# Optimization experiments

Measured on AMD Instinct MI355X. Metric: run time of the kernel, lower is better.

The kernel has to match this reference:

```python
import jax, jax.numpy as jnp
import numpy as np

B, S, D = 8, 2048, 512
H, LAT, OUT = 8, 64, 64


def setup_inputs() -> dict:
    key = jax.random.key(0)
    ks = jax.random.split(key, 5)
    return {
        "x": jax.random.normal(ks[0], (B, S, D), dtype=jnp.float32),
        "WQ": jax.random.normal(ks[1], (H, D, LAT), dtype=jnp.float32) * 0.05,
        "WK": jax.random.normal(ks[2], (H, D, LAT), dtype=jnp.float32) * 0.05,
        "WV": jax.random.normal(ks[3], (H, D, OUT), dtype=jnp.float32) * 0.05,
        "WO": jax.random.normal(ks[4], (H * OUT, OUT), dtype=jnp.float32) * 0.05,
    }


def reference(x, WQ, WK, WV, WO):
    # Per-head projections, vectorized over heads (faithful to the TF python loop).
    Q = jnp.einsum('bsd,hdk->bhsk', x, WQ)   # [B,H,S,LAT]
    K = jnp.einsum('bsd,hdk->bhsk', x, WK)   # [B,H,S,LAT]
    V = jnp.einsum('bsd,hdo->bhso', x, WV)   # [B,H,S,OUT]
    scale = jnp.asarray(1.0 / np.sqrt(LAT), dtype=x.dtype)
    A = jnp.einsum('bhqk,bhsk->bhqs', Q, K) * scale  # [B,H,S,S]
    A = jax.nn.softmax(A, axis=-1)
    O = jnp.einsum('bhqs,bhso->bhqo', A, V)  # [B,H,S,OUT]
    # concat heads along last axis (head 0 first, matching the TF loop order)
    O = jnp.transpose(O, (0, 2, 1, 3)).reshape(x.shape[0], x.shape[1], H * OUT)
    return O @ WO  # [B,S,OUT]
```

## Files before the change

### kernel.cpp

```cpp
#include <hip/hip_runtime.h>
#include <hip/hip_bf16.h>
#include <math.h>

static constexpr int Bn = 8, Sn = 2048, Dn = 512, Hn = 8, LATn = 64, OUTn = 64;

typedef short  bf16x8 __attribute__((ext_vector_type(8)));
typedef float  f32x4  __attribute__((ext_vector_type(4)));

__device__ __forceinline__ unsigned short f2bf(float f) {
    union { float f; unsigned int i; } v; v.f = f;
    unsigned int x = v.i;
    return (unsigned short)((x + 0x7FFFu + ((x >> 16) & 1u)) >> 16);
}
__device__ __forceinline__ unsigned int pack2bf(float a, float b) {
    unsigned int ua = __float_as_uint(a) + 0x8000u;
    unsigned int ub = __float_as_uint(b) + 0x8000u;
    return (ua >> 16) | (ub & 0xFFFF0000u);
}

#if __has_builtin(__builtin_amdgcn_exp2f)
#define EXP2(x) __builtin_amdgcn_exp2f(x)
#else
#define EXP2(x) exp2f(x)
#endif

__device__ __forceinline__ void gl_lds16(const void* g, void* l) {
    __builtin_amdgcn_global_load_lds(
        (const __attribute__((address_space(1))) unsigned int*)g,
        (__attribute__((address_space(3))) unsigned int*)l, 16, 0, 0);
}

__global__ __launch_bounds__(256) void wprep(
    const float* __restrict__ WQ, const float* __restrict__ WK,
    const float* __restrict__ WV, const float* __restrict__ WO,
    unsigned short* __restrict__ WT)
{
    __shared__ float tile[64][65];
    const int t  = threadIdx.x;
    const int d0 = blockIdx.x * 64;
    const int yy = blockIdx.y;

    const float* W; float scale = 1.0f; size_t dstbase;
    if (yy < 24) {
        int h = yy / 3, which = yy % 3;
        W = (which == 0) ? WQ : (which == 1) ? WK : WV;
        W += (size_t)h * Dn * 64;
        if (which == 0) scale = 0.125f * 1.44269504088896f;
        dstbase = ((size_t)h * 192 + which * 64) * Dn;
    } else {
        W = WO;
        dstbase = (size_t)8 * 192 * Dn;
    }

    for (int i = 0; i < 4; ++i) {
        int idx = i * 256 + t;
        int r = idx >> 4, c = (idx & 15) * 4;
        float4 u = *(const float4*)(W + (size_t)(d0 + r) * 64 + c);
        tile[r][c] = u.x; tile[r][c+1] = u.y; tile[r][c+2] = u.z; tile[r][c+3] = u.w;
    }
    __syncthreads();
    const int n = t & 63, dd = t >> 6;
    unsigned short pk[16];
    for (int i = 0; i < 16; ++i) pk[i] = f2bf(tile[dd*16 + i][n] * scale);
    size_t dst = dstbase + (size_t)n * Dn + d0 + dd * 16;
    *(bf16x8*)(WT + dst)     = *(bf16x8*)(pk);
    *(bf16x8*)(WT + dst + 8) = *(bf16x8*)(pk + 8);
}

__global__ __launch_bounds__(256) void qkv_mfma(
    const float* __restrict__ x, const unsigned short* __restrict__ WT,
    unsigned short* __restrict__ Qb, unsigned short* __restrict__ Kb,
    unsigned short* __restrict__ VT)
{
    __shared__ __align__(16) unsigned short lds[64*72 + 192*72];
    unsigned short* Xs = lds;
    unsigned short* Ws = lds + 64*72;
    unsigned short* L  = lds;

    const int t  = threadIdx.x;
    const int w  = t >> 6, ln = t & 63;
    const int nl = ln & 15, g = ln >> 4;
    const int bh = blockIdx.y, b = bh >> 3, h = bh & 7;
    const int s0 = blockIdx.x * 64;

    f32x4 acc[4][3];
    for (int m = 0; m < 4; ++m)
        for (int j = 0; j < 3; ++j) acc[m][j] = (f32x4){0.f, 0.f, 0.f, 0.f};

    for (int k0 = 0; k0 < Dn; k0 += 64) {
        __syncthreads();
        for (int i = 0; i < 2; ++i) {
            int idx = i * 256 + t;
            int r = idx >> 3, c = (idx & 7) * 8;
            const float* src = x + ((size_t)(b * Sn + s0 + r)) * Dn + k0 + c;
            float4 u0 = *(const float4*)(src);
            float4 u1 = *(const float4*)(src + 4);
            unsigned int pk[4] = { pack2bf(u0.x, u0.y), pack2bf(u0.z, u0.w),
                                   pack2bf(u1.x, u1.y), pack2bf(u1.z, u1.w) };
            *(bf16x8*)(Xs + r*72 + c) = *(bf16x8*)pk;
        }
        for (int i = 0; i < 6; ++i) {
            int idx = i * 256 + t;
            int r = idx >> 3, c = (idx & 7) * 8;
            *(bf16x8*)(Ws + r*72 + c) =
                *(const bf16x8*)(WT + ((size_t)h * 192 + r) * Dn + k0 + c);
        }
        __syncthreads();
        #pragma unroll
        for (int kc = 0; kc < 2; ++kc) {
            bf16x8 a[4], bb[3];
            for (int m = 0; m < 4; ++m)
                a[m]  = *(const bf16x8*)(Xs + (16*m + nl)*72 + 32*kc + 8*g);
            for (int j = 0; j < 3; ++j)
                bb[j] = *(const bf16x8*)(Ws + ((3*w + j)*16 + nl)*72 + 32*kc + 8*g);
            for (int m = 0; m < 4; ++m)
                for (int j = 0; j < 3; ++j)
                    acc[m][j] = __builtin_amdgcn_mfma_f32_16x16x32_bf16(
                                    a[m], bb[j], acc[m][j], 0, 0, 0);
        }
    }
    __syncthreads();
    for (int m = 0; m < 4; ++m)
        for (int j = 0; j < 3; ++j) {
            int n = 48*w + 16*j + nl;
            for (int r = 0; r < 4; ++r)
                L[(16*m + 4*g + r)*200 + n] = f2bf(acc[m][j][r]);
        }
    __syncthreads();
    for (int i = 0; i < 4; ++i) {
        int idx = i * 256 + t;
        int r = idx >> 4, c = (idx & 15) * 8;
        bf16x8 v = *(const bf16x8*)(L + r*200 + c);
        size_t o = ((size_t)bh * Sn + s0 + r) * 64;
        if (c < 64) *(bf16x8*)(Qb + o + c)      = v;
        else        *(bf16x8*)(Kb + o + c - 64) = v;
    }
    {
        int o = t & 63, cc = t >> 6;
        unsigned short pk[16];
        for (int i = 0; i < 16; ++i) pk[i] = L[(16*cc + i)*200 + 128 + o];
        size_t dst = ((size_t)bh * 64 + o) * Sn + s0 + 16*cc;
        *(bf16x8*)(VT + dst)     = *(bf16x8*)(pk);
        *(bf16x8*)(VT + dst + 8) = *(bf16x8*)(pk + 8);
    }
}

__global__ __launch_bounds__(512, 2) void flash_mfma(
    const unsigned short* __restrict__ Qb,
    const unsigned short* __restrict__ Kb,
    const unsigned short* __restrict__ VT,
    unsigned short* __restrict__ Ob)
{
    __shared__ __align__(16) unsigned short KV[2][2][4096];
    __shared__ __align__(16) unsigned short Pt[8][4096];

    const int t  = threadIdx.x;
    const int w  = t >> 6, ln = t & 63;
    const int qh = ln & 15, g = (ln >> 4) & 3;
    const int bh = blockIdx.y, b = bh >> 3, h = bh & 7;
    const int q0 = blockIdx.x * 512;
    const int qw = q0 + 64 * w;

    bf16x8 bq[4][2];
    #pragma unroll
    for (int qs = 0; qs < 4; ++qs) {
        const unsigned short* qp =
            Qb + ((size_t)bh * Sn + qw + 16*qs + qh) * 64 + 8*g;
        bq[qs][0] = *(const bf16x8*)(qp);
        bq[qs][1] = *(const bf16x8*)(qp + 32);
    }

    const int r0 = t >> 3;
    const int cs = (t & 7) ^ (r0 & 7);
    const unsigned short* kg = Kb + ((size_t)bh * Sn + r0) * 64 + cs * 8;
    const unsigned short* vg = VT + ((size_t)bh * 64 + r0) * Sn + cs * 8;

    const int swz8  = (qh & 7) * 8;
    const int koff0 = qh*64 + (((g    ) ^ (qh & 7)) * 8);
    const int koff1 = qh*64 + (((4 + g) ^ (qh & 7)) * 8);

    f32x4 o_acc[4][4];
    #pragma unroll
    for (int qs = 0; qs < 4; ++qs)
        #pragma unroll
        for (int f = 0; f < 4; ++f) o_acc[qs][f] = (f32x4){0.f, 0.f, 0.f, 0.f};
    float l_run[4] = {0.f, 0.f, 0.f, 0.f};

    gl_lds16(kg, &KV[0][0][w * 512]);
    gl_lds16(vg, &KV[0][1][w * 512]);
    __syncthreads();

    int buf = 0;
    for (int kt = 0; kt < Sn / 64; ++kt) {
        if (kt < Sn / 64 - 1) {
            kg += 4096; vg += 64;
            gl_lds16(kg, &KV[buf ^ 1][0][w * 512]);
            gl_lds16(vg, &KV[buf ^ 1][1][w * 512]);
        }
        const unsigned short* Kt = KV[buf][0];
        const unsigned short* Vt = KV[buf][1];

        f32x4 st[4][4];
        #pragma unroll
        for (int qs = 0; qs < 4; ++qs)
            #pragma unroll
            for (int f = 0; f < 4; ++f) st[qs][f] = (f32x4){0.f, 0.f, 0.f, 0.f};
        #pragma unroll
        for (int kc = 0; kc < 2; ++kc) {
            const int ko = kc ? koff1 : koff0;
            bf16x8 a0 = *(const bf16x8*)(Kt + ko);
            bf16x8 a1 = *(const bf16x8*)(Kt + ko + 1024);
            bf16x8 a2 = *(const bf16x8*)(Kt + ko + 2048);
            bf16x8 a3 = *(const bf16x8*)(Kt + ko + 3072);
            #pragma unroll
            for (int qs = 0; qs < 4; ++qs) {
                st[qs][0] = __builtin_amdgcn_mfma_f32_16x16x32_bf16(a0, bq[qs][kc], st[qs][0], 0, 0, 0);
                st[qs][1] = __builtin_amdgcn_mfma_f32_16x16x32_bf16(a1, bq[qs][kc], st[qs][1], 0, 0, 0);
                st[qs][2] = __builtin_amdgcn_mfma_f32_16x16x32_bf16(a2, bq[qs][kc], st[qs][2], 0, 0, 0);
                st[qs][3] = __builtin_amdgcn_mfma_f32_16x16x32_bf16(a3, bq[qs][kc], st[qs][3], 0, 0, 0);
            }
        }

        #pragma unroll
        for (int qs = 0; qs < 4; ++qs) {
            float ls = 0.f;
            unsigned short* pw = Pt[w] + qs*1024 + qh*64;
            #pragma unroll
            for (int f = 0; f < 4; ++f) {
                float p0 = EXP2(st[qs][f][0]);
                float p1 = EXP2(st[qs][f][1]);
                float p2 = EXP2(st[qs][f][2]);
                float p3 = EXP2(st[qs][f][3]);
                ls += (p0 + p1) + (p2 + p3);
                *(uint2*)(pw + ((16*f + 4*g) ^ swz8)) =
                    make_uint2(pack2bf(p0, p1), pack2bf(p2, p3));
            }
            ls += __shfl_xor(ls, 16);
            ls += __shfl_xor(ls, 32);
            l_run[qs] += ls;
        }

        #pragma unroll
        for (int kc = 0; kc < 2; ++kc) {
            const int ko = kc ? koff1 : koff0;
            bf16x8 v0 = *(const bf16x8*)(Vt + ko);
            bf16x8 v1 = *(const bf16x8*)(Vt + ko + 1024);
            bf16x8 v2 = *(const bf16x8*)(Vt + ko + 2048);
            bf16x8 v3 = *(const bf16x8*)(Vt + ko + 3072);
            #pragma unroll
            for (int qs = 0; qs < 4; ++qs) {
                bf16x8 bp = *(const bf16x8*)(Pt[w] + qs*1024 + qh*64
                                             + ((32*kc + 8*g) ^ swz8));
                o_acc[qs][0] = __builtin_amdgcn_mfma_f32_16x16x32_bf16(v0, bp, o_acc[qs][0], 0, 0, 0);
                o_acc[qs][1] = __builtin_amdgcn_mfma_f32_16x16x32_bf16(v1, bp, o_acc[qs][1], 0, 0, 0);
                o_acc[qs][2] = __builtin_amdgcn_mfma_f32_16x16x32_bf16(v2, bp, o_acc[qs][2], 0, 0, 0);
                o_acc[qs][3] = __builtin_amdgcn_mfma_f32_16x16x32_bf16(v3, bp, o_acc[qs][3], 0, 0, 0);
            }
        }

        __syncthreads();
        buf ^= 1;
    }

    #pragma unroll
    for (int qs = 0; qs < 4; ++qs) {
        float inv_l = 1.f / l_run[qs];
        unsigned short* op = Ob
            + ((size_t)(b * Sn + q0 + 64*w + 16*qs + qh)) * 512 + h*64 + 4*g;
        #pragma unroll
        for (int f = 0; f < 4; ++f) {
            unsigned int lo = pack2bf(o_acc[qs][f][0] * inv_l, o_acc[qs][f][1] * inv_l);
            unsigned int hi = pack2bf(o_acc[qs][f][2] * inv_l, o_acc[qs][f][3] * inv_l);
            *(uint2*)(op + 16*f) = make_uint2(lo, hi);
        }
    }
}

__global__ __launch_bounds__(256) void out_mfma(
    const unsigned short* __restrict__ Ob, const unsigned short* __restrict__ WOT,
    float* __restrict__ out)
{
    __shared__ __align__(16) unsigned short As[64 * 72];
    __shared__ __align__(16) unsigned short Bs[64 * 72];

    const int t  = threadIdx.x;
    const int w  = t >> 6, ln = t & 63;
    const int qh = ln & 15, g = ln >> 4;
    const int bs0 = blockIdx.x * 64;

    f32x4 acc[4];
    for (int n = 0; n < 4; ++n) acc[n] = (f32x4){0.f, 0.f, 0.f, 0.f};

    for (int k0 = 0; k0 < 512; k0 += 64) {
        __syncthreads();
        for (int i = 0; i < 2; ++i) {
            int idx = i * 256 + t;
            int r = idx >> 3, c = (idx & 7) * 8;
            *(bf16x8*)(As + r*72 + c) =
                *(const bf16x8*)(Ob + ((size_t)(bs0 + r)) * 512 + k0 + c);
            *(bf16x8*)(Bs + r*72 + c) =
                *(const bf16x8*)(WOT + (size_t)r * Dn + k0 + c);
        }
        __syncthreads();
        #pragma unroll
        for (int kc = 0; kc < 2; ++kc) {
            bf16x8 a = *(const bf16x8*)(As + (16*w + qh)*72 + 32*kc + 8*g);
            #pragma unroll
            for (int n = 0; n < 4; ++n) {
                bf16x8 bb = *(const bf16x8*)(Bs + (16*n + qh)*72 + 32*kc + 8*g);
                acc[n] = __builtin_amdgcn_mfma_f32_16x16x32_bf16(a, bb, acc[n], 0, 0, 0);
            }
        }
    }
    for (int n = 0; n < 4; ++n)
        for (int r = 0; r < 4; ++r)
            out[((size_t)(bs0 + 16*w + 4*g + r)) * 64 + 16*n + qh] = acc[n][r];
}

extern "C" void kernel_launch(void* const* d_in, const int* in_sizes, int n_in,
                              void* d_out, int out_size, void* d_ws, size_t ws_size,
                              hipStream_t stream)
{
    const float* x  = (const float*)d_in[0];
    const float* WQ = (const float*)d_in[1];
    const float* WK = (const float*)d_in[2];
    const float* WV = (const float*)d_in[3];
    const float* WO = (const float*)d_in[4];
    float* out = (float*)d_out;

    const size_t NQ = (size_t)Bn * Hn * Sn * LATn;
    char* p = (char*)d_ws;
    unsigned short* Qb  = (unsigned short*)p;           p += NQ * 2;
    unsigned short* Kb  = (unsigned short*)p;           p += NQ * 2;
    unsigned short* VT  = (unsigned short*)p;           p += NQ * 2;
    unsigned short* WT  = (unsigned short*)p;           p += ((size_t)Hn*192*Dn + 64*Dn) * 2;
    unsigned short* Ob  = (unsigned short*)p;
    unsigned short* WOT = WT + (size_t)Hn * 192 * Dn;

    wprep     <<<dim3(8, 25),         256, 0, stream>>>(WQ, WK, WV, WO, WT);
    qkv_mfma  <<<dim3(Sn/64, Bn*Hn),  256, 0, stream>>>(x, WT, Qb, Kb, VT);
    flash_mfma<<<dim3(Sn/512, Bn*Hn), 512, 0, stream>>>(Qb, Kb, VT, Ob);
    out_mfma  <<<dim3(Bn*Sn/64),      256, 0, stream>>>(Ob, WOT, out);
}
```

Measured before the change: 223.0 us.

## Keep P in registers by permuting V row layout, shrink flash blocks to 256

The score accumulator layout from the QK MFMA is fed straight into the PV MFMA as the B operand, which removes the per-tile LDS round trip for P (the Pt buffer). To make that valid, the VT transpose in the QKV kernel permutes the key order within each 64-key tile to match the register layout. Per-tile row-sum shuffles move out of the loop to a single reduction at the end. Flash blocks shrink from 512 to 256 threads, with each thread loading two K/V chunks per tile, which doubles the number of blocks and the K/V traffic per query.

```diff
diff --git a/kernel.cpp b/kernel.cpp
--- a/kernel.cpp
+++ b/kernel.cpp
@@ -138,27 +138,29 @@
     {
         int o = t & 63, cc = t >> 6;
         unsigned short pk[16];
-        for (int i = 0; i < 16; ++i) pk[i] = L[(16*cc + i)*200 + 128 + o];
+        for (int i = 0; i < 16; ++i) {
+            int srow = 32*(cc>>1) + 16*((i>>2)&1) + 8*(cc&1) + 4*((i>>3)&1) + (i&3);
+            pk[i] = L[srow*200 + 128 + o];
+        }
         size_t dst = ((size_t)bh * 64 + o) * Sn + s0 + 16*cc;
         *(bf16x8*)(VT + dst)     = *(bf16x8*)(pk);
         *(bf16x8*)(VT + dst + 8) = *(bf16x8*)(pk + 8);
     }
 }
 
-__global__ __launch_bounds__(512, 2) void flash_mfma(
+__global__ __launch_bounds__(256, 2) void flash_mfma(
     const unsigned short* __restrict__ Qb,
     const unsigned short* __restrict__ Kb,
     const unsigned short* __restrict__ VT,
     unsigned short* __restrict__ Ob)
 {
     __shared__ __align__(16) unsigned short KV[2][2][4096];
-    __shared__ __align__(16) unsigned short Pt[8][4096];
 
     const int t  = threadIdx.x;
     const int w  = t >> 6, ln = t & 63;
     const int qh = ln & 15, g = (ln >> 4) & 3;
     const int bh = blockIdx.y, b = bh >> 3, h = bh & 7;
-    const int q0 = blockIdx.x * 512;
+    const int q0 = blockIdx.x * 256;
     const int qw = q0 + 64 * w;
 
     bf16x8 bq[4][2];
@@ -170,12 +172,15 @@
         bq[qs][1] = *(const bf16x8*)(qp + 32);
     }
 
-    const int r0 = t >> 3;
-    const int cs = (t & 7) ^ (r0 & 7);
-    const unsigned short* kg = Kb + ((size_t)bh * Sn + r0) * 64 + cs * 8;
-    const unsigned short* vg = VT + ((size_t)bh * 64 + r0) * Sn + cs * 8;
-
-    const int swz8  = (qh & 7) * 8;
+    const int r0a = t >> 3;
+    const int csa = (t & 7) ^ (r0a & 7);
+    const int r0b = 32 + (t >> 3);
+    const int csb = (t & 7) ^ (r0b & 7);
+    const unsigned short* kga = Kb + ((size_t)bh * Sn + r0a) * 64 + csa * 8;
+    const unsigned short* kgb = Kb + ((size_t)bh * Sn + r0b) * 64 + csb * 8;
+    const unsigned short* vga = VT + ((size_t)bh * 64 + r0a) * Sn + csa * 8;
+    const unsigned short* vgb = VT + ((size_t)bh * 64 + r0b) * Sn + csb * 8;
+
     const int koff0 = qh*64 + (((g    ) ^ (qh & 7)) * 8);
     const int koff1 = qh*64 + (((4 + g) ^ (qh & 7)) * 8);
 
@@ -186,16 +191,20 @@
         for (int f = 0; f < 4; ++f) o_acc[qs][f] = (f32x4){0.f, 0.f, 0.f, 0.f};
     float l_run[4] = {0.f, 0.f, 0.f, 0.f};
 
-    gl_lds16(kg, &KV[0][0][w * 512]);
-    gl_lds16(vg, &KV[0][1][w * 512]);
+    gl_lds16(kga, &KV[0][0][w * 512]);
+    gl_lds16(kgb, &KV[0][0][2048 + w * 512]);
+    gl_lds16(vga, &KV[0][1][w * 512]);
+    gl_lds16(vgb, &KV[0][1][2048 + w * 512]);
     __syncthreads();
 
     int buf = 0;
     for (int kt = 0; kt < Sn / 64; ++kt) {
         if (kt < Sn / 64 - 1) {
-            kg += 4096; vg += 64;
-            gl_lds16(kg, &KV[buf ^ 1][0][w * 512]);
-            gl_lds16(vg, &KV[buf ^ 1][1][w * 512]);
+            kga += 4096; kgb += 4096; vga += 64; vgb += 64;
+            gl_lds16(kga, &KV[buf ^ 1][0][w * 512]);
+            gl_lds16(kgb, &KV[buf ^ 1][0][2048 + w * 512]);
+            gl_lds16(vga, &KV[buf ^ 1][1][w * 512]);
+            gl_lds16(vgb, &KV[buf ^ 1][1][2048 + w * 512]);
         }
         const unsigned short* Kt = KV[buf][0];
         const unsigned short* Vt = KV[buf][1];
@@ -221,23 +230,25 @@
             }
         }
 
+        bf16x8 bp[4][2];
         #pragma unroll
         for (int qs = 0; qs < 4; ++qs) {
-            float ls = 0.f;
-            unsigned short* pw = Pt[w] + qs*1024 + qh*64;
-            #pragma unroll
-            for (int f = 0; f < 4; ++f) {
-                float p0 = EXP2(st[qs][f][0]);
-                float p1 = EXP2(st[qs][f][1]);
-                float p2 = EXP2(st[qs][f][2]);
-                float p3 = EXP2(st[qs][f][3]);
-                ls += (p0 + p1) + (p2 + p3);
-                *(uint2*)(pw + ((16*f + 4*g) ^ swz8)) =
-                    make_uint2(pack2bf(p0, p1), pack2bf(p2, p3));
+            float e0[4], e1[4], e2[4], e3[4];
+            #pragma unroll
+            for (int r = 0; r < 4; ++r) {
+                e0[r] = EXP2(st[qs][0][r]);
+                e1[r] = EXP2(st[qs][1][r]);
+                e2[r] = EXP2(st[qs][2][r]);
+                e3[r] = EXP2(st[qs][3][r]);
             }
-            ls += __shfl_xor(ls, 16);
-            ls += __shfl_xor(ls, 32);
-            l_run[qs] += ls;
+            l_run[qs] += ((e0[0]+e0[1])+(e0[2]+e0[3])) + ((e1[0]+e1[1])+(e1[2]+e1[3]))
+                       + ((e2[0]+e2[1])+(e2[2]+e2[3])) + ((e3[0]+e3[1])+(e3[2]+e3[3]));
+            unsigned int p0[4] = { pack2bf(e0[0],e0[1]), pack2bf(e0[2],e0[3]),
+                                   pack2bf(e1[0],e1[1]), pack2bf(e1[2],e1[3]) };
+            unsigned int p1[4] = { pack2bf(e2[0],e2[1]), pack2bf(e2[2],e2[3]),
+                                   pack2bf(e3[0],e3[1]), pack2bf(e3[2],e3[3]) };
+            bp[qs][0] = *(bf16x8*)p0;
+            bp[qs][1] = *(bf16x8*)p1;
         }
 
         #pragma unroll
@@ -249,17 +260,21 @@
             bf16x8 v3 = *(const bf16x8*)(Vt + ko + 3072);
             #pragma unroll
             for (int qs = 0; qs < 4; ++qs) {
-                bf16x8 bp = *(const bf16x8*)(Pt[w] + qs*1024 + qh*64
-                                             + ((32*kc + 8*g) ^ swz8));
-                o_acc[qs][0] = __builtin_amdgcn_mfma_f32_16x16x32_bf16(v0, bp, o_acc[qs][0], 0, 0, 0);
-                o_acc[qs][1] = __builtin_amdgcn_mfma_f32_16x16x32_bf16(v1, bp, o_acc[qs][1], 0, 0, 0);
-                o_acc[qs][2] = __builtin_amdgcn_mfma_f32_16x16x32_bf16(v2, bp, o_acc[qs][2], 0, 0, 0);
-                o_acc[qs][3] = __builtin_amdgcn_mfma_f32_16x16x32_bf16(v3, bp, o_acc[qs][3], 0, 0, 0);
+                o_acc[qs][0] = __builtin_amdgcn_mfma_f32_16x16x32_bf16(v0, bp[qs][kc], o_acc[qs][0], 0, 0, 0);
+                o_acc[qs][1] = __builtin_amdgcn_mfma_f32_16x16x32_bf16(v1, bp[qs][kc], o_acc[qs][1], 0, 0, 0);
+                o_acc[qs][2] = __builtin_amdgcn_mfma_f32_16x16x32_bf16(v2, bp[qs][kc], o_acc[qs][2], 0, 0, 0);
+                o_acc[qs][3] = __builtin_amdgcn_mfma_f32_16x16x32_bf16(v3, bp[qs][kc], o_acc[qs][3], 0, 0, 0);
             }
         }
 
         __syncthreads();
         buf ^= 1;
+    }
+
+    #pragma unroll
+    for (int qs = 0; qs < 4; ++qs) {
+        l_run[qs] += __shfl_xor(l_run[qs], 16);
+        l_run[qs] += __shfl_xor(l_run[qs], 32);
     }
 
     #pragma unroll
@@ -339,6 +354,6 @@
 
     wprep     <<<dim3(8, 25),         256, 0, stream>>>(WQ, WK, WV, WO, WT);
     qkv_mfma  <<<dim3(Sn/64, Bn*Hn),  256, 0, stream>>>(x, WT, Qb, Kb, VT);
-    flash_mfma<<<dim3(Sn/512, Bn*Hn), 512, 0, stream>>>(Qb, Kb, VT, Ob);
+    flash_mfma<<<dim3(Sn/256, Bn*Hn), 256, 0, stream>>>(Qb, Kb, VT, Ob);
     out_mfma  <<<dim3(Bn*Sn/64),      256, 0, stream>>>(Ob, WOT, out);
 }
```

Measured after the change: 207.1 us. 7.1% less time.
